# Kernel optimization log

Measured on AMD Instinct MI355X. Metric: run time of the kernel, lower is better.

Reference implementation:

```python
import jax, jax.numpy as jnp
import numpy as np
from functools import partial

D_MODEL = 1024
D_STATE = 16
D_CONV = 4
EXPAND = 2
DIM = EXPAND * D_MODEL  # 2048


def setup_inputs() -> dict:
    key = jax.random.key(0)
    ks = jax.random.split(key, 10)
    s = lambda fan_in: 1.0 / np.sqrt(fan_in)
    inp = {
        "x": jax.random.normal(ks[0], (8, 2048, D_MODEL), dtype=jnp.float32),
        "W_in": jax.random.normal(ks[1], (DIM, D_MODEL), dtype=jnp.float32) * s(D_MODEL),
        "b_in": jnp.zeros((DIM,), dtype=jnp.float32),
        "conv_w": jax.random.normal(ks[2], (DIM, 1, D_CONV), dtype=jnp.float32) * s(D_CONV),
        "conv_b": jnp.zeros((DIM,), dtype=jnp.float32),
        "W_x": jax.random.normal(ks[3], (3 * D_STATE, DIM), dtype=jnp.float32) * s(DIM),
        "W_dt": jax.random.normal(ks[4], (DIM, D_STATE), dtype=jnp.float32) * s(D_STATE),
        "b_dt": jnp.zeros((DIM,), dtype=jnp.float32),
        "W_out": jax.random.normal(ks[5], (D_MODEL, DIM), dtype=jnp.float32) * s(DIM),
        "b_out": jnp.zeros((D_MODEL,), dtype=jnp.float32),
    }
    return inp


def _selective_scan(xc, delta, A, Bm, Cm):
    # xc, delta: (B, L, DIM); Bm, Cm: (B, L, N); A: (N,)
    Bsz = xc.shape[0]
    h0 = jnp.zeros((Bsz, DIM, D_STATE), dtype=xc.dtype)

    def step(h, inputs):
        xc_t, d_t, b_t, c_t = inputs  # (B,DIM),(B,DIM),(B,N),(B,N)
        h = h * jnp.exp(d_t[:, :, None] * A) + xc_t[:, :, None] * b_t[:, None, :]
        y_t = jnp.einsum("bdn,bn->bd", h, c_t)
        return h, y_t

    tm = lambda a: jnp.swapaxes(a, 0, 1)  # time-major
    _, ys = jax.lax.scan(step, h0, (tm(xc), tm(delta), tm(Bm), tm(Cm)))
    return jnp.swapaxes(ys, 0, 1)  # (B, L, DIM)


def reference(x, W_in, b_in, conv_w, conv_b, W_x, W_dt, b_dt, W_out, b_out):
    A = -jnp.exp(jnp.linspace(0.0, -5.0, D_STATE).astype(x.dtype))  # (N,)
    xp = x @ W_in.T + b_in  # (B, L, DIM)
    # depthwise conv1d, padding=D_CONV-1 on BOTH sides (as torch Conv1d) -> length L+D_CONV-1
    xc = jax.lax.conv_general_dilated(
        jnp.swapaxes(xp, 1, 2), conv_w,
        window_strides=(1,), padding=[(D_CONV - 1, D_CONV - 1)],
        feature_group_count=DIM,
        dimension_numbers=("NCH", "OIH", "NCH"),
    ) + conv_b[None, :, None]
    xc = jnp.swapaxes(xc, 1, 2)  # (B, Lc, DIM)
    x_dbl = xc @ W_x.T  # (B, Lc, 3N)
    d_raw, Bm, Cm = jnp.split(x_dbl, [D_STATE, 2 * D_STATE], axis=-1)
    delta = jax.nn.softplus(d_raw @ W_dt.T + b_dt)  # (B, Lc, DIM)
    y = _selective_scan(xc, delta, A, Bm, Cm)  # (B, Lc, DIM)
    return y @ W_out.T + b_out  # (B, Lc, D_MODEL)
```

## Files before the change

kernel.cpp:

```cpp
#include <hip/hip_runtime.h>
#include <cstdint>
#include <cstddef>

#define B8 8
#define LSEQ 2048
#define LC 2051
#define DMODEL 1024
#define DIM 2048
#define LPAD 2054
#define M2 16408
#define M2P 16512
#define CS 32
#define NCH 65

typedef __attribute__((ext_vector_type(8))) short short8;
typedef __attribute__((ext_vector_type(4))) float floatx4;
typedef __attribute__((ext_vector_type(2))) float float2v;
typedef __attribute__((address_space(3))) unsigned short lds_ushort;

__device__ __constant__ float AeT[16] = {
  -1.0f,          -0.71653131f, -0.51341712f, -0.36787944f,
  -0.26359714f,   -0.18887560f, -0.13533528f, -0.09697208f,
  -0.06948345f,   -0.04978707f, -0.03567399f, -0.02556154f,
  -0.01831564f,   -0.01312373f, -0.00940356f, -0.00673795f};

#define LOG2E 1.44269504088896f

__device__ __forceinline__ float bf2f(unsigned short h) {
  union { unsigned int u; float f; } v; v.u = ((unsigned int)h) << 16; return v.f;
}
__device__ __forceinline__ unsigned short f2bf(float f) {
  union { float f; unsigned int u; } v; v.f = f;
  unsigned int r = (v.u + 0x7FFFu + ((v.u >> 16) & 1u)) >> 16;
  return (unsigned short)r;
}

__device__ __forceinline__ float2v pk_mul_vv(float2v a, float2v b) {
  float2v d; asm("v_pk_mul_f32 %0, %1, %2" : "=v"(d) : "v"(a), "v"(b)); return d;
}
__device__ __forceinline__ float2v pk_mul_sv(float2v bs, float2v a) {
  float2v d; asm("v_pk_mul_f32 %0, %1, %2" : "=v"(d) : "s"(bs), "v"(a)); return d;
}
__device__ __forceinline__ float2v pk_fma_vvv(float2v a, float2v b, float2v c) {
  float2v d; asm("v_pk_fma_f32 %0, %1, %2, %3" : "=v"(d) : "v"(a), "v"(b), "v"(c)); return d;
}
__device__ __forceinline__ float2v pk_fma_vsv(float2v a, float2v bs, float2v c) {
  float2v d; asm("v_pk_fma_f32 %0, %1, %2, %3" : "=v"(d) : "v"(a), "s"(bs), "v"(c)); return d;
}
__device__ __forceinline__ float2v pk_add_vv(float2v a, float2v b) {
  float2v d; asm("v_pk_add_f32 %0, %1, %2" : "=v"(d) : "v"(a), "v"(b)); return d;
}
__device__ __forceinline__ float exp2_raw(float x) {
  float d; asm("v_exp_f32 %0, %1" : "=v"(d) : "v"(x)); return d;
}

__device__ __forceinline__ short8 ds_read_b128_(const lds_ushort* p) {
  floatx4 d;
  unsigned addr = (unsigned)(size_t)p;
  asm volatile("ds_read_b128 %0, %1" : "=v"(d) : "v"(addr));
  return __builtin_bit_cast(short8, d);
}

__global__ __launch_bounds__(256) void init_kernel(const float* __restrict__ x,
                                                   const float* __restrict__ W_in,
                                                   const float* __restrict__ W_out,
                                                   const float* __restrict__ W_x,
                                                   unsigned short* __restrict__ xA,
                                                   unsigned short* __restrict__ wInB,
                                                   unsigned short* __restrict__ wOutB,
                                                   unsigned short* __restrict__ wXB,
                                                   unsigned short* __restrict__ xp) {
  const int gid = blockIdx.x;
  const float* in; unsigned short* out; int i;
  if (gid < 8192)        { in = x;     out = xA;    i = gid * 256 + threadIdx.x; }
  else if (gid < 9216)   { in = W_in;  out = wInB;  i = (gid - 8192) * 256 + threadIdx.x; }
  else if (gid < 10240)  { in = W_out; out = wOutB; i = (gid - 9216) * 256 + threadIdx.x; }
  else if (gid < 10288)  { in = W_x;   out = wXB;   i = (gid - 10240) * 256 + threadIdx.x; }
  else {
    int ii = (gid - 10288) * 256 + threadIdx.x;
    int b = ii / 1536;
    int r6 = (ii % 1536) / 256;
    int dd = (ii % 256) * 8;
    int row = (r6 < 3) ? r6 : (2048 + r6);
    *(uint4*)(xp + ((size_t)b * LPAD + row) * DIM + dd) = make_uint4(0, 0, 0, 0);
    return;
  }
  const float4* p = (const float4*)in + (size_t)i * 2;
  float4 a = p[0], b = p[1];
  uint4 o;
  o.x = (unsigned)f2bf(a.x) | ((unsigned)f2bf(a.y) << 16);
  o.y = (unsigned)f2bf(a.z) | ((unsigned)f2bf(a.w) << 16);
  o.z = (unsigned)f2bf(b.x) | ((unsigned)f2bf(b.y) << 16);
  o.w = (unsigned)f2bf(b.z) | ((unsigned)f2bf(b.w) << 16);
  *((uint4*)out + i) = o;
}

__global__ __launch_bounds__(256) void conv_kernel(const unsigned short* __restrict__ xp,
                                                   const float* __restrict__ conv_w,
                                                   const float* __restrict__ conv_b,
                                                   unsigned short* __restrict__ xc) {
  const int tc0 = blockIdx.x * 16;
  const int b = blockIdx.y;
  const int d0 = threadIdx.x * 8;

  float4 cw[8];
#pragma unroll
  for (int j = 0; j < 8; ++j) cw[j] = *(const float4*)(conv_w + (size_t)(d0 + j) * 4);
  float cb[8];
  {
    const float4* cb4 = (const float4*)(conv_b + d0);
    float4 c0 = cb4[0], c1 = cb4[1];
    cb[0] = c0.x; cb[1] = c0.y; cb[2] = c0.z; cb[3] = c0.w;
    cb[4] = c1.x; cb[5] = c1.y; cb[6] = c1.z; cb[7] = c1.w;
  }

  const unsigned short* base = xp + ((size_t)b * LPAD + tc0) * DIM + d0;
  unsigned short* outp = xc + ((size_t)b * LC + tc0) * DIM + d0;

  auto loadrow = [&](float (&w)[8], int r) {
    uint4 v = *(const uint4*)(base + (size_t)r * DIM);
    w[0] = bf2f(v.x & 0xffff); w[1] = bf2f(v.x >> 16);
    w[2] = bf2f(v.y & 0xffff); w[3] = bf2f(v.y >> 16);
    w[4] = bf2f(v.z & 0xffff); w[5] = bf2f(v.z >> 16);
    w[6] = bf2f(v.w & 0xffff); w[7] = bf2f(v.w >> 16);
  };

  float wa[8], wb[8], wc[8];
  loadrow(wa, 0); loadrow(wb, 1); loadrow(wc, 2);
#pragma unroll
  for (int i = 0; i < 16; ++i) {
    float wd[8];
    loadrow(wd, i + 3);
    if (tc0 + i < LC) {
      float acc[8];
#pragma unroll
      for (int j = 0; j < 8; ++j) {
        acc[j] = cb[j];
        acc[j] = fmaf(wa[j], cw[j].x, acc[j]);
        acc[j] = fmaf(wb[j], cw[j].y, acc[j]);
        acc[j] = fmaf(wc[j], cw[j].z, acc[j]);
        acc[j] = fmaf(wd[j], cw[j].w, acc[j]);
      }
      uint4 o;
      o.x = (unsigned)f2bf(acc[0]) | ((unsigned)f2bf(acc[1]) << 16);
      o.y = (unsigned)f2bf(acc[2]) | ((unsigned)f2bf(acc[3]) << 16);
      o.z = (unsigned)f2bf(acc[4]) | ((unsigned)f2bf(acc[5]) << 16);
      o.w = (unsigned)f2bf(acc[6]) | ((unsigned)f2bf(acc[7]) << 16);
      *(uint4*)(outp + (size_t)i * DIM) = o;
    }
#pragma unroll
    for (int j = 0; j < 8; ++j) { wa[j] = wb[j]; wb[j] = wc[j]; wc[j] = wd[j]; }
  }
}

#define GAS(p) ((const __attribute__((address_space(1))) void*)(p))
#define LAS(p) ((__attribute__((address_space(3))) void*)(p))

template <int MODE, int NBM, int NBN, int LX, int TAIL, int SPLITK>
__global__ __launch_bounds__(256) void gemm_bt(const unsigned short* __restrict__ A,
                                               const unsigned short* __restrict__ Bw,
                                               const float* __restrict__ bias,
                                               void* __restrict__ Cout, int K) {
  const int gid = blockIdx.x;
  const int mainBlocks = 8 * LX * NBN;
  int bm, bn, ks = 0;
  if constexpr (SPLITK) {
    ks = gid & 7;
    bm = gid >> 3;
    bn = 0;
  } else if (TAIL && gid >= mainBlocks) {
    const int e = gid - mainBlocks;
    bm = 8 * LX + e / NBN;
    bn = e % NBN;
  } else {
    const int xcd = gid & 7;
    const int j = gid >> 3;
    bm = xcd * LX + (j % LX);
    bn = j / LX;
  }
  if (bm >= NBM) return;

  __shared__ __align__(16) unsigned short As[2][128 * 64];
  __shared__ __align__(16) unsigned short Bs[2][128 * 64];
  const int tid = threadIdx.x;
  const int lane = tid & 63, wave = tid >> 6;
  const int wr = wave >> 1, wc = wave & 1;

  floatx4 acc[4][4];
#pragma unroll
  for (int i = 0; i < 4; ++i)
#pragma unroll
    for (int j2 = 0; j2 < 4; ++j2) acc[i][j2] = (floatx4){0.f, 0.f, 0.f, 0.f};

  const int srow = tid >> 3;
  const int scol = ((tid & 7) ^ ((tid >> 3) & 7)) * 8;
  const unsigned short* Ab[4];
  const unsigned short* Bb[4];
#pragma unroll
  for (int L = 0; L < 4; ++L) {
    Ab[L] = A  + (size_t)(bm * 128 + L * 32 + srow) * K + scol;
    Bb[L] = Bw + (size_t)(bn * 128 + L * 32 + srow) * K + scol;
  }

  const int fr = lane & 15;
  const int hi = lane >> 4;
  const int fx = fr & 7;

  auto STAGE = [&](int buf, int k0) {
#pragma unroll
    for (int L = 0; L < 4; ++L) {
      __builtin_amdgcn_global_load_lds(GAS(Ab[L] + k0), LAS(&As[buf][L * 2048 + tid * 8]), 16, 0, 0);
      __builtin_amdgcn_global_load_lds(GAS(Bb[L] + k0), LAS(&Bs[buf][L * 2048 + tid * 8]), 16, 0, 0);
    }
  };

  const int kbase = SPLITK ? ks * (K >> 3) : 0;
  const int NT = (SPLITK ? (K >> 3) : K) >> 6;
  STAGE(0, kbase);
  asm volatile("s_waitcnt vmcnt(0)");
  __syncthreads();

  int cur = 0;
  for (int t = 0; t < NT; ++t) {
    if (t + 1 < NT) STAGE(cur ^ 1, kbase + (t + 1) * 64);

    const lds_ushort* tA = (const lds_ushort*)LAS(&As[cur][0]);
    const lds_ushort* tB = (const lds_ushort*)LAS(&Bs[cur][0]);
#pragma unroll
    for (int kk = 0; kk < 2; ++kk) {
      const int pb = ((kk * 4 + hi) ^ fx) * 8;
      short8 af[4], bf[4];
#pragma unroll
      for (int mt = 0; mt < 4; ++mt) af[mt] = ds_read_b128_(tA + (wr * 64 + mt * 16 + fr) * 64 + pb);
#pragma unroll
      for (int nt = 0; nt < 4; ++nt) bf[nt] = ds_read_b128_(tB + (wc * 64 + nt * 16 + fr) * 64 + pb);
      asm volatile("s_waitcnt lgkmcnt(0)");
      __builtin_amdgcn_sched_barrier(0);
      __builtin_amdgcn_s_setprio(1);
#pragma unroll
      for (int mt = 0; mt < 4; ++mt)
#pragma unroll
        for (int nt = 0; nt < 4; ++nt)
          acc[mt][nt] = __builtin_amdgcn_mfma_f32_16x16x32_bf16(af[mt], bf[nt], acc[mt][nt], 0, 0, 0);
      __builtin_amdgcn_s_setprio(0);
    }
    __syncthreads();
    cur ^= 1;
  }

  const int er = (lane >> 4) * 4, ec = lane & 15;
#pragma unroll
  for (int mt = 0; mt < 4; ++mt) {
#pragma unroll
    for (int nt = 0; nt < 4; ++nt) {
#pragma unroll
      for (int i = 0; i < 4; ++i) {
        int r = bm * 128 + wr * 64 + mt * 16 + er + i;
        int c = bn * 128 + wc * 64 + nt * 16 + ec;
        float v = acc[mt][nt][i];
        if constexpr (MODE == 0) {
          int bb = r >> 11, t = r & 2047;
          ((unsigned short*)Cout)[((size_t)bb * LPAD + 3 + t) * DIM + c] = f2bf(v + bias[c]);
        } else if constexpr (MODE == 1) {
          if (c < 48) ((float*)Cout)[((size_t)ks * M2P + r) * 48 + c] = v;
        } else {
          if (r < M2) ((float*)Cout)[(size_t)r * DMODEL + c] = v + bias[c];
        }
      }
    }
  }
}

__global__ __launch_bounds__(256) void reduce_xdbl(const float* __restrict__ part,
                                                   float* __restrict__ xdbl) {
  int i = blockIdx.x * 256 + threadIdx.x;
  if (i >= 196896) return;
  float4 s = make_float4(0.f, 0.f, 0.f, 0.f);
#pragma unroll
  for (int ks = 0; ks < 8; ++ks) {
    float4 v = *(const float4*)(part + (size_t)ks * M2P * 48 + (size_t)i * 4);
    s.x += v.x; s.y += v.y; s.z += v.z; s.w += v.w;
  }
  *(float4*)(xdbl + (size_t)i * 4) = s;
}

__global__ __launch_bounds__(256) void delta_kernel(const float* __restrict__ xdbl,
                                                    const float* __restrict__ W_dt,
                                                    const float* __restrict__ b_dt,
                                                    unsigned short* __restrict__ delta) {
  const int d = blockIdx.y * 256 + threadIdx.x;
  const int r0 = blockIdx.x * 8;
  float wv[16];
  const float4* wp = (const float4*)(W_dt + (size_t)d * 16);
#pragma unroll
  for (int q = 0; q < 4; ++q) {
    float4 t = wp[q];
    wv[q * 4 + 0] = t.x; wv[q * 4 + 1] = t.y; wv[q * 4 + 2] = t.z; wv[q * 4 + 3] = t.w;
  }
  const float bd = b_dt[d];
#pragma unroll
  for (int j = 0; j < 8; ++j) {
    const float* dr = xdbl + (size_t)(r0 + j) * 48;
    float z0 = bd, z1 = 0.f, z2 = 0.f, z3 = 0.f;
#pragma unroll
    for (int n = 0; n < 16; n += 4) {
      z0 = fmaf(dr[n + 0], wv[n + 0], z0);
      z1 = fmaf(dr[n + 1], wv[n + 1], z1);
      z2 = fmaf(dr[n + 2], wv[n + 2], z2);
      z3 = fmaf(dr[n + 3], wv[n + 3], z3);
    }
    float z = (z0 + z1) + (z2 + z3);
    float dl = (z > 20.f) ? z : __logf(1.f + __expf(z));
    delta[(size_t)(r0 + j) * DIM + d] = f2bf(dl);
  }
}

__global__ __launch_bounds__(256) void scan_pass1(const unsigned short* __restrict__ xc,
                                                  const unsigned short* __restrict__ dl,
                                                  const float* __restrict__ xd,
                                                  unsigned short* __restrict__ sdbuf,
                                                  unsigned short* __restrict__ qbuf) {
  const int wid = __builtin_amdgcn_readfirstlane((int)(threadIdx.x >> 6));
  const int lane = threadIdx.x & 63;
  const int W = blockIdx.x * 4 + wid;
  const int dg = W & 31;
  const int rest = W >> 5;
  const int c = rest % NCH;
  const int b = rest / NCH;
  const int d = dg * 64 + lane;
  const int t0 = c * CS;
  const int nst = (t0 + CS <= LC) ? CS : (LC - t0);

  float2v A2L[8];
#pragma unroll
  for (int i = 0; i < 8; ++i)
    A2L[i] = (float2v){AeT[2 * i] * LOG2E, AeT[2 * i + 1] * LOG2E};

  float2v h2[8];
#pragma unroll
  for (int i = 0; i < 8; ++i) h2[i] = (float2v){0.f, 0.f};
  float sumd = 0.f;

  const size_t row0 = (size_t)b * LC + t0;
  const float* xdb = xd + row0 * 48 + 16;
  const unsigned short* xcp = xc + row0 * DIM + d;
  const unsigned short* dp  = dl + row0 * DIM + d;

  auto body = [&](int s) {
    float2v Bv[8];
#pragma unroll
    for (int j = 0; j < 8; ++j) Bv[j] = *(const float2v*)(xdb + (size_t)s * 48 + 2 * j);
    float dlt = bf2f(dp[(size_t)s * DIM]);
    float xcv = bf2f(xcp[(size_t)s * DIM]);
    sumd += dlt;
    float2v dlt2 = (float2v){dlt, dlt};
    float2v xcv2 = (float2v){xcv, xcv};
#pragma unroll
    for (int i = 0; i < 8; ++i) {
      float2v arg = pk_mul_vv(dlt2, A2L[i]);
      float e0 = exp2_raw(arg.x), e1 = exp2_raw(arg.y);
      float2v e2 = (float2v){e0, e1};
      h2[i] = pk_fma_vvv(h2[i], e2, pk_mul_sv(Bv[i], xcv2));
    }
  };

  if (nst == CS) {
#pragma unroll
    for (int s = 0; s < CS; ++s) body(s);
  } else {
    for (int s = 0; s < nst; ++s) body(s);
  }

  sdbuf[((size_t)(b * NCH + c) << 11) + d] = f2bf(sumd);
  const size_t base = ((size_t)(b * NCH + c) * 16) * 2048 + d;
#pragma unroll
  for (int i = 0; i < 8; ++i) {
    qbuf[base + ((size_t)(2 * i) << 11)]     = f2bf(h2[i].x);
    qbuf[base + ((size_t)(2 * i + 1) << 11)] = f2bf(h2[i].y);
  }
}

__global__ __launch_bounds__(256) void scan_boundary(const unsigned short* __restrict__ sdbuf,
                                                     unsigned short* __restrict__ qbuf) {
  const int tid = threadIdx.x;
  const int n = tid >> 4;
  const int d = blockIdx.x * 16 + (tid & 15);
  const int b = blockIdx.y;
  const float aL = AeT[n] * LOG2E;
  float h = 0.f;
  for (int c = 0; c < NCH; ++c) {
    const size_t sbase = ((size_t)(b * NCH + c) << 11);
    const float sd = bf2f(sdbuf[sbase + d]);
    const size_t base = (sbase << 4) + ((size_t)n << 11) + d;
    const float qv = bf2f(qbuf[base]);
    const float Pv = exp2_raw(sd * aL);
    qbuf[base] = f2bf(h);
    h = fmaf(Pv, h, qv);
  }
}

__global__ __launch_bounds__(256) void scan_pass2(const unsigned short* __restrict__ xc,
                                                  const unsigned short* __restrict__ dl,
                                                  const float* __restrict__ xd,
                                                  const unsigned short* __restrict__ hinit,
                                                  unsigned short* __restrict__ y) {
  const int wid = __builtin_amdgcn_readfirstlane((int)(threadIdx.x >> 6));
  const int lane = threadIdx.x & 63;
  const int W = blockIdx.x * 4 + wid;
  const int dg = W & 31;
  const int rest = W >> 5;
  const int c = rest % NCH;
  const int b = rest / NCH;
  const int d = dg * 64 + lane;
  const int t0 = c * CS;
  const int nst = (t0 + CS <= LC) ? CS : (LC - t0);

  float2v A2L[8];
#pragma unroll
  for (int i = 0; i < 8; ++i)
    A2L[i] = (float2v){AeT[2 * i] * LOG2E, AeT[2 * i + 1] * LOG2E};

  const size_t base = ((size_t)(b * NCH + c) * 16) * 2048 + d;
  float2v h2[8];
#pragma unroll
  for (int i = 0; i < 8; ++i)
    h2[i] = (float2v){bf2f(hinit[base + ((size_t)(2 * i) << 11)]),
                      bf2f(hinit[base + ((size_t)(2 * i + 1) << 11)])};

  const size_t row0 = (size_t)b * LC + t0;
  const float* xdb = xd + row0 * 48 + 16;
  const unsigned short* xcp = xc + row0 * DIM + d;
  const unsigned short* dp  = dl + row0 * DIM + d;
  unsigned short* yp = y + row0 * DIM + d;

  auto body = [&](int s) {
    float2v Bv[8], Cv[8];
#pragma unroll
    for (int j = 0; j < 8; ++j) {
      Bv[j] = *(const float2v*)(xdb + (size_t)s * 48 + 2 * j);
      Cv[j] = *(const float2v*)(xdb + (size_t)s * 48 + 16 + 2 * j);
    }
    float dlt = bf2f(dp[(size_t)s * DIM]);
    float xcv = bf2f(xcp[(size_t)s * DIM]);
    float2v dlt2 = (float2v){dlt, dlt};
    float2v xcv2 = (float2v){xcv, xcv};
    float2v y2[4];
#pragma unroll
    for (int i = 0; i < 4; ++i) y2[i] = (float2v){0.f, 0.f};
#pragma unroll
    for (int i = 0; i < 8; ++i) {
      float2v arg = pk_mul_vv(dlt2, A2L[i]);
      float e0 = exp2_raw(arg.x), e1 = exp2_raw(arg.y);
      float2v e2 = (float2v){e0, e1};
      h2[i] = pk_fma_vvv(h2[i], e2, pk_mul_sv(Bv[i], xcv2));
      y2[i & 3] = pk_fma_vsv(h2[i], Cv[i], y2[i & 3]);
    }
    float2v s01 = pk_add_vv(y2[0], y2[1]);
    float2v s23 = pk_add_vv(y2[2], y2[3]);
    float2v st = pk_add_vv(s01, s23);
    yp[(size_t)s * DIM] = f2bf(st.x + st.y);
  };

  if (nst == CS) {
#pragma unroll
    for (int s = 0; s < CS; ++s) body(s);
  } else {
    for (int s = 0; s < nst; ++s) body(s);
  }
}

extern "C" void kernel_launch(void* const* d_in, const int* in_sizes, int n_in,
                              void* d_out, int out_size, void* d_ws, size_t ws_size,
                              hipStream_t stream) {
  const float* x      = (const float*)d_in[0];
  const float* W_in   = (const float*)d_in[1];
  const float* b_in   = (const float*)d_in[2];
  const float* conv_w = (const float*)d_in[3];
  const float* conv_b = (const float*)d_in[4];
  const float* W_x    = (const float*)d_in[5];
  const float* W_dt   = (const float*)d_in[6];
  const float* b_dt   = (const float*)d_in[7];
  const float* W_out  = (const float*)d_in[8];
  const float* b_out  = (const float*)d_in[9];

  char* w = (char*)d_ws;
  unsigned short* xp    = (unsigned short*)w;
  unsigned short* delta = (unsigned short*)w;
  unsigned short* ybuf  = (unsigned short*)w;
  size_t off = (size_t)M2P * DIM * 2;
  unsigned short* xcb  = (unsigned short*)(w + off); off += (size_t)M2P * DIM * 2;
  size_t xA_off = off;
  unsigned short* xA   = (unsigned short*)(w + off); off += (size_t)16384 * 1024 * 2;
  unsigned short* wInB = (unsigned short*)(w + off); off += (size_t)2048 * 1024 * 2;
  unsigned short* wOutB= (unsigned short*)(w + off); off += (size_t)1024 * 2048 * 2;
  unsigned short* wXB  = (unsigned short*)(w + off); off += (size_t)128 * 2048 * 2;
  float* xdbl          = (float*)(w + off);          off += (size_t)M2 * 48 * 4;
  float* part           = (float*)(w + xA_off);
  unsigned short* sdbuf = (unsigned short*)(w + xA_off);
  unsigned short* qbuf  = (unsigned short*)(w + xA_off + (size_t)B8 * NCH * 2048 * 2);
  (void)ws_size; (void)in_sizes; (void)n_in; (void)out_size;

  init_kernel<<<10336, 256, 0, stream>>>(x, W_in, W_out, W_x, xA, wInB, wOutB, wXB, xp);

  gemm_bt<0, 128, 16, 16, 0, 0><<<2048, 256, 0, stream>>>(xA, wInB, b_in, xp, 1024);
  conv_kernel<<<dim3(129, B8), 256, 0, stream>>>(xp, conv_w, conv_b, xcb);
  gemm_bt<1, 129, 1, 0, 0, 1><<<1032, 256, 0, stream>>>(xcb, wXB, nullptr, part, 2048);
  reduce_xdbl<<<770, 256, 0, stream>>>(part, xdbl);
  delta_kernel<<<dim3(2051, 8), 256, 0, stream>>>(xdbl, W_dt, b_dt, delta);

  scan_pass1<<<4160, 256, 0, stream>>>(xcb, delta, xdbl, sdbuf, qbuf);
  scan_boundary<<<dim3(128, B8), 256, 0, stream>>>(sdbuf, qbuf);
  scan_pass2<<<4160, 256, 0, stream>>>(xcb, delta, xdbl, qbuf, ybuf);

  gemm_bt<2, 129, 8, 16, 1, 0><<<1032, 256, 0, stream>>>(ybuf, wOutB, b_out, (float*)d_out, 2048);
}
```

Measured before the change: 511.3 us.

## Add 256x256-tile 8-wave GEMM with phased LDS pipeline for in/out projections

Adds a new GEMM kernel that uses 256x256 output tiles, 512 threads and 8 waves, each wave computing 128x64. It splits K staging into half-tiles interleaved with MFMA phases, using explicit barriers and vmcnt waits to overlap global-to-LDS loads with compute. The input and output projection GEMMs now use this kernel, while the split-K x_dbl GEMM keeps the old kernel with its MODE 0/2 paths removed. The larger tiles raise arithmetic intensity and cut redundant operand loads, at the cost of heavy register pressure (32 accumulators per wave), one block per CU, and fewer blocks (260) for the output GEMM, which may leave CUs idle on the tail.

```diff
diff --git a/kernel.cpp b/kernel.cpp
--- a/kernel.cpp
+++ b/kernel.cpp
@@ -162,13 +162,111 @@
                                                const float* __restrict__ bias,
                                                void* __restrict__ Cout, int K) {
   const int gid = blockIdx.x;
-  const int mainBlocks = 8 * LX * NBN;
   int bm, bn, ks = 0;
   if constexpr (SPLITK) {
     ks = gid & 7;
     bm = gid >> 3;
     bn = 0;
-  } else if (TAIL && gid >= mainBlocks) {
+  } else {
+    const int xcd = gid & 7;
+    const int j = gid >> 3;
+    bm = xcd * LX + (j % LX);
+    bn = j / LX;
+  }
+  if (bm >= NBM) return;
+
+  __shared__ __align__(16) unsigned short As[2][128 * 64];
+  __shared__ __align__(16) unsigned short Bs[2][128 * 64];
+  const int tid = threadIdx.x;
+  const int lane = tid & 63, wave = tid >> 6;
+  const int wr = wave >> 1, wc = wave & 1;
+
+  floatx4 acc[4][4];
+#pragma unroll
+  for (int i = 0; i < 4; ++i)
+#pragma unroll
+    for (int j2 = 0; j2 < 4; ++j2) acc[i][j2] = (floatx4){0.f, 0.f, 0.f, 0.f};
+
+  const int srow = tid >> 3;
+  const int scol = ((tid & 7) ^ ((tid >> 3) & 7)) * 8;
+  const unsigned short* Ab[4];
+  const unsigned short* Bb[4];
+#pragma unroll
+  for (int L = 0; L < 4; ++L) {
+    Ab[L] = A  + (size_t)(bm * 128 + L * 32 + srow) * K + scol;
+    Bb[L] = Bw + (size_t)(bn * 128 + L * 32 + srow) * K + scol;
+  }
+
+  const int fr = lane & 15;
+  const int hi = lane >> 4;
+  const int fx = fr & 7;
+
+  auto STAGE = [&](int buf, int k0) {
+#pragma unroll
+    for (int L = 0; L < 4; ++L) {
+      __builtin_amdgcn_global_load_lds(GAS(Ab[L] + k0), LAS(&As[buf][L * 2048 + tid * 8]), 16, 0, 0);
+      __builtin_amdgcn_global_load_lds(GAS(Bb[L] + k0), LAS(&Bs[buf][L * 2048 + tid * 8]), 16, 0, 0);
+    }
+  };
+
+  const int kbase = SPLITK ? ks * (K >> 3) : 0;
+  const int NT = (SPLITK ? (K >> 3) : K) >> 6;
+  STAGE(0, kbase);
+  asm volatile("s_waitcnt vmcnt(0)");
+  __syncthreads();
+
+  int cur = 0;
+  for (int t = 0; t < NT; ++t) {
+    if (t + 1 < NT) STAGE(cur ^ 1, kbase + (t + 1) * 64);
+    const lds_ushort* tA = (const lds_ushort*)LAS(&As[cur][0]);
+    const lds_ushort* tB = (const lds_ushort*)LAS(&Bs[cur][0]);
+#pragma unroll
+    for (int kk = 0; kk < 2; ++kk) {
+      const int pb = ((kk * 4 + hi) ^ fx) * 8;
+      short8 af[4], bf[4];
+#pragma unroll
+      for (int mt = 0; mt < 4; ++mt) af[mt] = ds_read_b128_(tA + (wr * 64 + mt * 16 + fr) * 64 + pb);
+#pragma unroll
+      for (int nt = 0; nt < 4; ++nt) bf[nt] = ds_read_b128_(tB + (wc * 64 + nt * 16 + fr) * 64 + pb);
+      asm volatile("s_waitcnt lgkmcnt(0)");
+      __builtin_amdgcn_sched_barrier(0);
+#pragma unroll
+      for (int mt = 0; mt < 4; ++mt)
+#pragma unroll
+        for (int nt = 0; nt < 4; ++nt)
+          acc[mt][nt] = __builtin_amdgcn_mfma_f32_16x16x32_bf16(af[mt], bf[nt], acc[mt][nt], 0, 0, 0);
+    }
+    __syncthreads();
+    cur ^= 1;
+  }
+
+  const int er = (lane >> 4) * 4, ec = lane & 15;
+#pragma unroll
+  for (int mt = 0; mt < 4; ++mt) {
+#pragma unroll
+    for (int nt = 0; nt < 4; ++nt) {
+#pragma unroll
+      for (int i = 0; i < 4; ++i) {
+        int r = bm * 128 + wr * 64 + mt * 16 + er + i;
+        int c = bn * 128 + wc * 64 + nt * 16 + ec;
+        float v = acc[mt][nt][i];
+        if constexpr (MODE == 1) {
+          if (c < 48) ((float*)Cout)[((size_t)ks * M2P + r) * 48 + c] = v;
+        }
+      }
+    }
+  }
+}
+
+template <int MODE, int NBM, int NBN, int LX, int TAIL>
+__global__ __launch_bounds__(512, 1) void gemm256(const unsigned short* __restrict__ A,
+                                                  const unsigned short* __restrict__ Bw,
+                                                  const float* __restrict__ bias,
+                                                  void* __restrict__ Cout, int K) {
+  const int gid = blockIdx.x;
+  const int mainBlocks = 8 * LX * NBN;
+  int bm, bn;
+  if (TAIL && gid >= mainBlocks) {
     const int e = gid - mainBlocks;
     bm = 8 * LX + e / NBN;
     bn = e % NBN;
@@ -180,89 +278,132 @@
   }
   if (bm >= NBM) return;
 
-  __shared__ __align__(16) unsigned short As[2][128 * 64];
-  __shared__ __align__(16) unsigned short Bs[2][128 * 64];
+  __shared__ __align__(16) unsigned short lds[2][2][2][8192];
+
   const int tid = threadIdx.x;
-  const int lane = tid & 63, wave = tid >> 6;
-  const int wr = wave >> 1, wc = wave & 1;
-
-  floatx4 acc[4][4];
-#pragma unroll
-  for (int i = 0; i < 4; ++i)
-#pragma unroll
-    for (int j2 = 0; j2 < 4; ++j2) acc[i][j2] = (floatx4){0.f, 0.f, 0.f, 0.f};
-
-  const int srow = tid >> 3;
-  const int scol = ((tid & 7) ^ ((tid >> 3) & 7)) * 8;
-  const unsigned short* Ab[4];
-  const unsigned short* Bb[4];
-#pragma unroll
-  for (int L = 0; L < 4; ++L) {
-    Ab[L] = A  + (size_t)(bm * 128 + L * 32 + srow) * K + scol;
-    Bb[L] = Bw + (size_t)(bn * 128 + L * 32 + srow) * K + scol;
-  }
+  const int lane = tid & 63;
+  const int wid = tid >> 6;
+  const int wr = wid >> 2;
+  const int wc = wid & 3;
+
+  const int srow0 = tid >> 2;
+  const int slb   = (tid & 3) ^ ((tid >> 4) & 3);
+  const unsigned short* aR0 = A  + (size_t)(bm * 256 + srow0)       * K + slb * 8;
+  const unsigned short* aR1 = A  + (size_t)(bm * 256 + 128 + srow0) * K + slb * 8;
+  const unsigned short* bR0 = Bw + (size_t)(bn * 256 + srow0)       * K + slb * 8;
+  const unsigned short* bR1 = Bw + (size_t)(bn * 256 + 128 + srow0) * K + slb * 8;
 
   const int fr = lane & 15;
   const int hi = lane >> 4;
-  const int fx = fr & 7;
-
-  auto STAGE = [&](int buf, int k0) {
-#pragma unroll
-    for (int L = 0; L < 4; ++L) {
-      __builtin_amdgcn_global_load_lds(GAS(Ab[L] + k0), LAS(&As[buf][L * 2048 + tid * 8]), 16, 0, 0);
-      __builtin_amdgcn_global_load_lds(GAS(Bb[L] + k0), LAS(&Bs[buf][L * 2048 + tid * 8]), 16, 0, 0);
-    }
-  };
-
-  const int kbase = SPLITK ? ks * (K >> 3) : 0;
-  const int NT = (SPLITK ? (K >> 3) : K) >> 6;
-  STAGE(0, kbase);
-  asm volatile("s_waitcnt vmcnt(0)");
-  __syncthreads();
-
-  int cur = 0;
-  for (int t = 0; t < NT; ++t) {
-    if (t + 1 < NT) STAGE(cur ^ 1, kbase + (t + 1) * 64);
-
-    const lds_ushort* tA = (const lds_ushort*)LAS(&As[cur][0]);
-    const lds_ushort* tB = (const lds_ushort*)LAS(&Bs[cur][0]);
-#pragma unroll
-    for (int kk = 0; kk < 2; ++kk) {
-      const int pb = ((kk * 4 + hi) ^ fx) * 8;
-      short8 af[4], bf[4];
-#pragma unroll
-      for (int mt = 0; mt < 4; ++mt) af[mt] = ds_read_b128_(tA + (wr * 64 + mt * 16 + fr) * 64 + pb);
-#pragma unroll
-      for (int nt = 0; nt < 4; ++nt) bf[nt] = ds_read_b128_(tB + (wc * 64 + nt * 16 + fr) * 64 + pb);
-      asm volatile("s_waitcnt lgkmcnt(0)");
-      __builtin_amdgcn_sched_barrier(0);
-      __builtin_amdgcn_s_setprio(1);
-#pragma unroll
-      for (int mt = 0; mt < 4; ++mt)
-#pragma unroll
-        for (int nt = 0; nt < 4; ++nt)
-          acc[mt][nt] = __builtin_amdgcn_mfma_f32_16x16x32_bf16(af[mt], bf[nt], acc[mt][nt], 0, 0, 0);
-      __builtin_amdgcn_s_setprio(0);
-    }
-    __syncthreads();
-    cur ^= 1;
-  }
+  const int pb = hi ^ ((fr >> 2) & 3);
+  int offA[8], offB[4];
+#pragma unroll
+  for (int m = 0; m < 8; ++m) offA[m] = (wr * 128 + m * 16 + fr) * 32 + pb * 8;
+#pragma unroll
+  for (int n = 0; n < 4; ++n) offB[n] = (wc * 64 + n * 16 + fr) * 32 + pb * 8;
+
+  floatx4 acc[8][4];
+#pragma unroll
+  for (int m = 0; m < 8; ++m)
+#pragma unroll
+    for (int n = 0; n < 4; ++n) acc[m][n] = (floatx4){0.f, 0.f, 0.f, 0.f};
+
+#define STAGE_A(t, kk) {                                                                   \
+    unsigned short* db_ = &lds[(t) & 1][0][kk][0];                                         \
+    const int ko_ = (t) * 64 + (kk) * 32;                                                  \
+    __builtin_amdgcn_global_load_lds(GAS(aR0 + ko_), LAS(db_ + tid * 8), 16, 0, 0);        \
+    __builtin_amdgcn_global_load_lds(GAS(aR1 + ko_), LAS(db_ + 4096 + tid * 8), 16, 0, 0); \
+  }
+#define STAGE_B(t, kk) {                                                                   \
+    unsigned short* db_ = &lds[(t) & 1][1][kk][0];                                         \
+    const int ko_ = (t) * 64 + (kk) * 32;                                                  \
+    __builtin_amdgcn_global_load_lds(GAS(bR0 + ko_), LAS(db_ + tid * 8), 16, 0, 0);        \
+    __builtin_amdgcn_global_load_lds(GAS(bR1 + ko_), LAS(db_ + 4096 + tid * 8), 16, 0, 0); \
+  }
+#define MF(a, b, c) __builtin_amdgcn_mfma_f32_16x16x32_bf16(a, b, c, 0, 0, 0)
+#define PH(d, kk, mh, STG, VMC) {                                                          \
+    const lds_ushort* pA_ = (const lds_ushort*)LAS(&lds[d][0][kk][0]);                     \
+    short8 af0, af1, af2, af3;                                                             \
+    if (mh == 0) {                                                                         \
+      const lds_ushort* pB_ = (const lds_ushort*)LAS(&lds[d][1][kk][0]);                   \
+      bf0 = ds_read_b128_(pB_ + offB[0]);                                                  \
+      bf1 = ds_read_b128_(pB_ + offB[1]);                                                  \
+      bf2 = ds_read_b128_(pB_ + offB[2]);                                                  \
+      bf3 = ds_read_b128_(pB_ + offB[3]);                                                  \
+    }                                                                                      \
+    af0 = ds_read_b128_(pA_ + offA[(mh) * 4 + 0]);                                         \
+    af1 = ds_read_b128_(pA_ + offA[(mh) * 4 + 1]);                                         \
+    af2 = ds_read_b128_(pA_ + offA[(mh) * 4 + 2]);                                         \
+    af3 = ds_read_b128_(pA_ + offA[(mh) * 4 + 3]);                                         \
+    STG;                                                                                   \
+    VMC;                                                                                   \
+    __builtin_amdgcn_s_barrier();                                                          \
+    asm volatile("s_waitcnt lgkmcnt(0)" ::: "memory");                                     \
+    __builtin_amdgcn_sched_barrier(0);                                                     \
+    __builtin_amdgcn_s_setprio(1);                                                         \
+    acc[(mh)*4+0][0] = MF(af0, bf0, acc[(mh)*4+0][0]);                                     \
+    acc[(mh)*4+0][1] = MF(af0, bf1, acc[(mh)*4+0][1]);                                     \
+    acc[(mh)*4+0][2] = MF(af0, bf2, acc[(mh)*4+0][2]);                                     \
+    acc[(mh)*4+0][3] = MF(af0, bf3, acc[(mh)*4+0][3]);                                     \
+    acc[(mh)*4+1][0] = MF(af1, bf0, acc[(mh)*4+1][0]);                                     \
+    acc[(mh)*4+1][1] = MF(af1, bf1, acc[(mh)*4+1][1]);                                     \
+    acc[(mh)*4+1][2] = MF(af1, bf2, acc[(mh)*4+1][2]);                                     \
+    acc[(mh)*4+1][3] = MF(af1, bf3, acc[(mh)*4+1][3]);                                     \
+    acc[(mh)*4+2][0] = MF(af2, bf0, acc[(mh)*4+2][0]);                                     \
+    acc[(mh)*4+2][1] = MF(af2, bf1, acc[(mh)*4+2][1]);                                     \
+    acc[(mh)*4+2][2] = MF(af2, bf2, acc[(mh)*4+2][2]);                                     \
+    acc[(mh)*4+2][3] = MF(af2, bf3, acc[(mh)*4+2][3]);                                     \
+    acc[(mh)*4+3][0] = MF(af3, bf0, acc[(mh)*4+3][0]);                                     \
+    acc[(mh)*4+3][1] = MF(af3, bf1, acc[(mh)*4+3][1]);                                     \
+    acc[(mh)*4+3][2] = MF(af3, bf2, acc[(mh)*4+3][2]);                                     \
+    acc[(mh)*4+3][3] = MF(af3, bf3, acc[(mh)*4+3][3]);                                     \
+    __builtin_amdgcn_s_setprio(0);                                                         \
+    __builtin_amdgcn_s_barrier();                                                          \
+  }
+#define VM6 asm volatile("s_waitcnt vmcnt(6)" ::: "memory")
+#define VM0 asm volatile("s_waitcnt vmcnt(0)" ::: "memory")
+
+  const int NT = K >> 6;
+  const int NITER = NT >> 1;
+
+  STAGE_B(0, 0); STAGE_A(0, 0); STAGE_B(0, 1); STAGE_A(0, 1);
+  STAGE_B(1, 0); STAGE_A(1, 0); STAGE_B(1, 1);
+  VM6;
+  __builtin_amdgcn_s_barrier();
+
+  for (int i = 0; i < NITER; ++i) {
+    const int T1 = 2 * i + 1, T2 = 2 * i + 2, T3 = 2 * i + 3;
+    const bool last = (i == NITER - 1);
+    short8 bf0, bf1, bf2, bf3;
+    PH(0, 0, 0, STAGE_A(T1, 1), );
+    PH(0, 0, 1, if (!last) STAGE_B(T2, 0), );
+    PH(0, 1, 0, if (!last) STAGE_A(T2, 0), );
+    PH(0, 1, 1, if (!last) STAGE_B(T2, 1), if (last) { VM0; } else { VM6; });
+    PH(1, 0, 0, if (!last) STAGE_A(T2, 1), );
+    PH(1, 0, 1, if (!last) STAGE_B(T3, 0), );
+    PH(1, 1, 0, if (!last) STAGE_A(T3, 0), );
+    PH(1, 1, 1, if (!last) STAGE_B(T3, 1), if (!last) { VM6; });
+  }
+#undef PH
+#undef STAGE_A
+#undef STAGE_B
+#undef MF
+#undef VM6
+#undef VM0
 
   const int er = (lane >> 4) * 4, ec = lane & 15;
 #pragma unroll
-  for (int mt = 0; mt < 4; ++mt) {
-#pragma unroll
-    for (int nt = 0; nt < 4; ++nt) {
+  for (int m = 0; m < 8; ++m) {
+#pragma unroll
+    for (int n = 0; n < 4; ++n) {
 #pragma unroll
       for (int i = 0; i < 4; ++i) {
-        int r = bm * 128 + wr * 64 + mt * 16 + er + i;
-        int c = bn * 128 + wc * 64 + nt * 16 + ec;
-        float v = acc[mt][nt][i];
+        int r = bm * 256 + wr * 128 + m * 16 + er + i;
+        int c = bn * 256 + wc * 64 + n * 16 + ec;
+        float v = acc[m][n][i];
         if constexpr (MODE == 0) {
-          int bb = r >> 11, t = r & 2047;
-          ((unsigned short*)Cout)[((size_t)bb * LPAD + 3 + t) * DIM + c] = f2bf(v + bias[c]);
-        } else if constexpr (MODE == 1) {
-          if (c < 48) ((float*)Cout)[((size_t)ks * M2P + r) * 48 + c] = v;
+          int bb = r >> 11, tt = r & 2047;
+          ((unsigned short*)Cout)[((size_t)bb * LPAD + 3 + tt) * DIM + c] = f2bf(v + bias[c]);
         } else {
           if (r < M2) ((float*)Cout)[(size_t)r * DMODEL + c] = v + bias[c];
         }
@@ -502,7 +643,7 @@
 
   init_kernel<<<10336, 256, 0, stream>>>(x, W_in, W_out, W_x, xA, wInB, wOutB, wXB, xp);
 
-  gemm_bt<0, 128, 16, 16, 0, 0><<<2048, 256, 0, stream>>>(xA, wInB, b_in, xp, 1024);
+  gemm256<0, 64, 8, 8, 0><<<512, 512, 0, stream>>>(xA, wInB, b_in, xp, 1024);
   conv_kernel<<<dim3(129, B8), 256, 0, stream>>>(xp, conv_w, conv_b, xcb);
   gemm_bt<1, 129, 1, 0, 0, 1><<<1032, 256, 0, stream>>>(xcb, wXB, nullptr, part, 2048);
   reduce_xdbl<<<770, 256, 0, stream>>>(part, xdbl);
@@ -512,5 +653,5 @@
   scan_boundary<<<dim3(128, B8), 256, 0, stream>>>(sdbuf, qbuf);
   scan_pass2<<<4160, 256, 0, stream>>>(xcb, delta, xdbl, qbuf, ybuf);
 
-  gemm_bt<2, 129, 8, 16, 1, 0><<<1032, 256, 0, stream>>>(ybuf, wOutB, b_out, (float*)d_out, 2048);
-}
+  gemm256<2, 65, 4, 8, 1><<<260, 512, 0, stream>>>(ybuf, wOutB, b_out, (float*)d_out, 2048);
+}
```

Result: slower. 532.2 us (+4.1%).
